# Performance work log

Hardware: AMD Instinct MI355X
Metric: run time of the kernel (lower is better)

Reference implementation:

```python
import jax, jax.numpy as jnp
import numpy as np

H, W, D, EMB, CELL = 16, 16, 6, 32, 128


def mat2quat(m):
    # m: [..., 12] row-major flattened [R|t] (3x4). Branchless vectorized
    # version of the original per-element Python-loop mat2quat.
    trans = m[..., jnp.array([3, 7, 11])]
    m00, m01, m02 = m[..., 0], m[..., 1], m[..., 2]
    m10, m11, m12 = m[..., 4], m[..., 5], m[..., 6]
    m20, m21, m22 = m[..., 8], m[..., 9], m[..., 10]
    t0 = 1 + m00 - m11 - m22
    q0 = jnp.stack([t0, m01 + m10, m20 + m02, m12 - m21], -1)
    t1 = 1 - m00 + m11 - m22
    q1 = jnp.stack([m01 + m10, t1, m12 + m21, m20 - m02], -1)
    t2 = 1 - m00 - m11 + m22
    q2 = jnp.stack([m20 + m02, m12 + m21, t2, m01 - m10], -1)
    t3 = 1 + m00 + m11 + m22
    q3 = jnp.stack([m12 - m21, m20 - m02, m01 - m10, t3], -1)
    cneg, cA, cB = m22 < 0, m00 > m11, m00 < -m11
    t = jnp.where(cneg, jnp.where(cA, t0, t1), jnp.where(cB, t2, t3))
    q = jnp.where(cneg[..., None], jnp.where(cA[..., None], q0, q1),
                  jnp.where(cB[..., None], q2, q3))
    q = q * (0.5 / jnp.sqrt(t))[..., None]
    return jnp.concatenate([trans, q], -1)  # [..., 7]


def transform_pose(pose_o, pose_q):
    # relative pose: inv([R_o|t_o]) @ [R_q|t_q]; original runs under no_grad
    B, N = pose_o.shape[:2]
    aff = jnp.array([0., 0., 0., 1.], dtype=pose_o.dtype)
    mo = jnp.concatenate([pose_o, jnp.broadcast_to(aff, (B, N, 4))], -1).reshape(B, N, 4, 4)
    mq = jnp.concatenate([pose_q, jnp.broadcast_to(aff, (B, 1, 4))], -1).reshape(B, 1, 4, 4)
    mt = jnp.linalg.inv(mo) @ mq  # [B,N,4,4]
    return jax.lax.stop_gradient(mt.reshape(B, N, 16)[..., :12])


def _mlp(x, W1, b1, W2, b2):
    return jax.nn.relu(x @ W1 + b1) @ W2 + b2


def reference(view_cell, pose_o, pose_q, Wk1, bk1, Wk2, bk2,
              Wq1, bq1, Wq2, bq2, Wa1, ba1, Wa2, ba2):
    B, N = pose_o.shape[:2]
    pose_o_quat = mat2quat(pose_o)  # [B,N,7]
    pose_q_quat = mat2quat(pose_q)  # [B,1,7]
    hg, wg = jnp.meshgrid(jnp.linspace(-1., 1., H), jnp.linspace(-1., 1., W), indexing='ij')
    code_o = jnp.stack([hg, wg], -1).reshape(-1, 2)              # [H*W, 2]
    emb_o = _mlp(code_o, Wk1, bk1, Wk2, bk2)                     # [H*W, EMB], shared keys
    dg, hg2, wg2 = jnp.meshgrid(jnp.linspace(0., 1., D), jnp.linspace(-1., 1., H),
                                jnp.linspace(-1., 1., W), indexing='ij')
    code_q = jnp.stack([dg, hg2, wg2], -1).reshape(-1, 3)        # [Q,3], Q=D*H*W
    Q = code_q.shape[0]
    pose_trans = transform_pose(pose_o, pose_q).reshape(B * N, 12)
    inp_q = jnp.concatenate([
        jnp.broadcast_to(pose_trans[:, None, :], (B * N, Q, 12)),
        jnp.broadcast_to(code_q[None], (B * N, Q, 3))], -1)      # [BN,Q,15]
    emb_q = _mlp(inp_q, Wq1, bq1, Wq2, bq2)                      # [BN,Q,EMB]
    mask = jax.nn.sigmoid(_mlp(emb_q, Wa1, ba1, Wa2, ba2))       # [BN,Q,1]
    v = jnp.transpose(view_cell, (0, 2, 3, 1)).reshape(B * N, H * W, CELL)
    att = jax.nn.softmax(jnp.einsum('bqe,ke->bqk', emb_q, emb_o), axis=-1)
    vatt = jnp.einsum('bqk,bkc->bqc', att, v)                    # [BN,Q,CELL]
    fused = jax.nn.sigmoid((mask * vatt).reshape(B, N, Q, CELL).sum(1))  # 'ocm' fusion
    out = jnp.transpose(fused, (0, 2, 1)).reshape(B, CELL, D, H, W)
    return out, pose_o_quat, pose_q_quat


def setup_inputs():
    key = jax.random.key(0)
    ks = jax.random.split(key, 12)
    B, N = 32, 8

    def make_pose(k, shape):
        kq, kt = jax.random.split(k)
        q = jax.random.normal(kq, shape + (4,))
        q = q / jnp.linalg.norm(q, axis=-1, keepdims=True)
        w, x, y, z = q[..., 0], q[..., 1], q[..., 2], q[..., 3]
        R = jnp.stack([1 - 2 * (y * y + z * z), 2 * (x * y - w * z), 2 * (x * z + w * y),
                       2 * (x * y + w * z), 1 - 2 * (x * x + z * z), 2 * (y * z - w * x),
                       2 * (x * z - w * y), 2 * (y * z + w * x), 1 - 2 * (x * x + y * y)],
                      -1).reshape(shape + (3, 3))
        t = jax.random.normal(kt, shape + (3, 1))
        return jnp.concatenate([R, t], -1).reshape(shape + (12,))

    def glorot(k, shp):
        return jax.random.normal(k, shp) * (1.0 / np.sqrt(shp[0]))

    return dict(
        view_cell=jax.random.normal(ks[0], (B * N, CELL, H, W)),
        pose_o=make_pose(ks[1], (B, N)),
        pose_q=make_pose(ks[2], (B, 1)),
        Wk1=glorot(ks[3], (2, 128)), bk1=jnp.zeros(128),
        Wk2=glorot(ks[4], (128, EMB)), bk2=jnp.zeros(EMB),
        Wq1=glorot(ks[5], (15, 256)), bq1=jnp.zeros(256),
        Wq2=glorot(ks[6], (256, EMB)), bq2=jnp.zeros(EMB),
        Wa1=glorot(ks[7], (EMB, 64)), ba1=jnp.zeros(64),
        Wa2=glorot(ks[8], (64, 1)), ba2=jnp.zeros(1),
    )
```

## Files before the change

kernel.cpp:

```cpp
#include <hip/hip_runtime.h>
#include <hip/hip_bf16.h>

using bf16 = __hip_bfloat16;
typedef __bf16 bfrag __attribute__((ext_vector_type(8)));
typedef float  ffrag __attribute__((ext_vector_type(4)));

#define WS_EO    0
#define WS_W2T   16384
#define WS_W1T   32768
#define WS_WA1T  49152
#define WS_VBF   65536

__device__ __forceinline__ float sigmoidf_(float x){ return 1.f/(1.f+__expf(-x)); }

__device__ __forceinline__ void relpose(const float* mo, const float* mq, float* o) {
  float a=mo[0],bb=mo[1],c=mo[2], d=mo[4],e=mo[5],f=mo[6], g=mo[8],h=mo[9],i9=mo[10];
  float A = e*i9-f*h, Bc = f*g-d*i9, C = d*h-e*g;
  float inv = 1.f/(a*A + bb*Bc + c*C);
  float r00=A*inv,  r01=(c*h-bb*i9)*inv, r02=(bb*f-c*e)*inv;
  float r10=Bc*inv, r11=(a*i9-c*g)*inv,  r12=(c*d-a*f)*inv;
  float r20=C*inv,  r21=(bb*g-a*h)*inv,  r22=(a*e-bb*d)*inv;
  float tx = mq[3]-mo[3], ty = mq[7]-mo[7], tz = mq[11]-mo[11];
  o[0]=r00*mq[0]+r01*mq[4]+r02*mq[8];  o[1]=r00*mq[1]+r01*mq[5]+r02*mq[9];
  o[2]=r00*mq[2]+r01*mq[6]+r02*mq[10]; o[3]=r00*tx+r01*ty+r02*tz;
  o[4]=r10*mq[0]+r11*mq[4]+r12*mq[8];  o[5]=r10*mq[1]+r11*mq[5]+r12*mq[9];
  o[6]=r10*mq[2]+r11*mq[6]+r12*mq[10]; o[7]=r10*tx+r11*ty+r12*tz;
  o[8]=r20*mq[0]+r21*mq[4]+r22*mq[8];  o[9]=r20*mq[1]+r21*mq[5]+r22*mq[9];
  o[10]=r20*mq[2]+r21*mq[6]+r22*mq[10]; o[11]=r20*tx+r21*ty+r22*tz;
}

__device__ __forceinline__ void quat7(const float* m, float* o) {
  float m00=m[0], m01=m[1], m02=m[2];
  float m10=m[4], m11=m[5], m12=m[6];
  float m20=m[8], m21=m[9], m22=m[10];
  float t,q0,q1,q2,q3;
  if (m22 < 0.f) {
    if (m00 > m11) { t=1.f+m00-m11-m22; q0=t;        q1=m01+m10; q2=m20+m02; q3=m12-m21; }
    else           { t=1.f-m00+m11-m22; q0=m01+m10; q1=t;        q2=m12+m21; q3=m20-m02; }
  } else {
    if (m00 < -m11){ t=1.f-m00-m11+m22; q0=m20+m02; q1=m12+m21; q2=t;        q3=m01-m10; }
    else           { t=1.f+m00+m11+m22; q0=m12-m21; q1=m20-m02; q2=m01-m10; q3=t;        }
  }
  float s = 0.5f / sqrtf(t);
  o[0]=m[3]; o[1]=m[7]; o[2]=m[11];
// ... 50 lines not shown
      for (int u=0;u<8;u++) {
        float4 w = *(const float4*)&Wk2[j*32+u*4];
        acc[u*4+0] = fmaf(hj, w.x, acc[u*4+0]);
        acc[u*4+1] = fmaf(hj, w.y, acc[u*4+1]);
        acc[u*4+2] = fmaf(hj, w.z, acc[u*4+2]);
        acc[u*4+3] = fmaf(hj, w.w, acc[u*4+3]);
      }
    }
    #pragma unroll
    for (int e=0;e<32;e++) ws_eo[k*32+e] = __float2bfloat16(acc[e]);
  } else if (role == 2) {
    int k = tid;
    #pragma unroll
    for (int u=0;u<8;u++) {
      float4 w = *(const float4*)&Wq2[k*32+u*4];
      ws_w2t[(u*4+0)*256+k] = __float2bfloat16(w.x);
      ws_w2t[(u*4+1)*256+k] = __float2bfloat16(w.y);
      ws_w2t[(u*4+2)*256+k] = __float2bfloat16(w.z);
      ws_w2t[(u*4+3)*256+k] = __float2bfloat16(w.w);
    }
  } else if (role == 3) {
    int h = tid;
    bf16 row[32];
    #pragma unroll
    for (int i=0;i<15;i++) row[i] = __float2bfloat16(Wq1[i*256+h]);
    row[15] = __float2bfloat16(bq1[h]);
    #pragma unroll
    for (int i=16;i<32;i++) row[i] = __float2bfloat16(0.f);
    #pragma unroll
    for (int i=0;i<32;i++) ws_w1t[h*32+i] = row[i];
  } else {
    if (tid < 64) {
      #pragma unroll
      for (int e=0;e<32;e++) ws_wa1t[tid*32+e] = __float2bfloat16(Wa1[e*64+tid]);
    }
  }
}

template<bool PRE>
__global__ void __launch_bounds__(256, 3)
k_main(const float* __restrict__ vc, const bf16* __restrict__ vbf_,
       const float* __restrict__ pose_o, const float* __restrict__ pose_q,
       const bf16* __restrict__ ws_eo_, const bf16* __restrict__ ws_w2t_,
       const bf16* __restrict__ ws_w1t_, const bf16* __restrict__ ws_wa1t_,
       const float* __restrict__ bq2,
       const float* __restrict__ ba1, const float* __restrict__ Wa2,
       const float* __restrict__ ba2,
       float* __restrict__ out) {
  __shared__ __align__(16) __bf16 s_h[32*264];
  __shared__ __align__(16) __bf16 s_p[32*264];
  __shared__ __align__(16) __bf16 s_eqT[32*40];
  __shared__ float s_pt[8][12];
  __shared__ float s_bw[128];
  __shared__ float s_redA[2][16][4];
  __shared__ float s_redB[2][16][4];
  __shared__ float s_redC[2][16][4];

  const __bf16* vbf  = (const __bf16*)vbf_;
  const __bf16* eo   = (const __bf16*)ws_eo_;
  const __bf16* w2t  = (const __bf16*)ws_w2t_;
  const __bf16* w1t  = (const __bf16*)ws_w1t_;
  const __bf16* wa1t = (const __bf16*)ws_wa1t_;

  const int tid  = threadIdx.x;
  const int w    = tid >> 6;
  const int lane = tid & 63;
  const int quad = lane >> 4;
  const int l15  = lane & 15;
  const int b    = blockIdx.y;
  const int qt0  = blockIdx.x * 32;

  if (tid < 8) {
    float mo[12], mq[12], pt[12];
    #pragma unroll
    for (int i=0;i<12;i++) mo[i] = pose_o[(b*8+tid)*12+i];
    #pragma unroll
    for (int i=0;i<12;i++) mq[i] = pose_q[b*12+i];
    relpose(mo, mq, pt);
    #pragma unroll
    for (int i=0;i<12;i++) s_pt[tid][i] = pt[i];
  }
  if (tid < 64) s_bw[tid] = ba1[tid];
  else if (tid < 128) s_bw[tid] = Wa2[tid-64];
  __syncthreads();

  bfrag w1A[4], eoA[4], waA;
  #pragma unroll
  for (int t=0;t<4;t++) {
    w1A[t] = *(const bfrag*)&w1t[((w*4+t)*16+l15)*32 + quad*8];
    eoA[t] = *(const bfrag*)&eo[((w*4+t)*16+l15)*32 + quad*8];
  }
  waA = *(const bfrag*)&wa1t[(w*16+l15)*32 + quad*8];
  const int   qs2 = w & 1, et = w >> 1;
  const float bq2v = bq2[et*16 + l15];
  float ba1r[4], wa2r[4];
  #pragma unroll
  for (int r=0;r<4;r++) { ba1r[r] = s_bw[w*16+quad*4+r]; wa2r[r] = s_bw[64+w*16+quad*4+r]; }
  const float ba2v = ba2[0];
  float c012[2][3];
  #pragma unroll
  for (int qs=0;qs<2;qs++) {
    int qg = qt0 + qs*16 + l15;
    c012[qs][0] = (float)(qg>>8) * 0.2f;
    c012[qs][1] = -1.f + (float)((qg>>4)&15)*(2.f/15.f);
    c012[qs][2] = -1.f + (float)(qg&15)*(2.f/15.f);
  }

  float acc[2][2][4];
  #pragma unroll
  for (int ct=0;ct<2;ct++)
    #pragma unroll
    for (int qs=0;qs<2;qs++)
      #pragma unroll
      for (int r=0;r<4;r++) acc[ct][qs][r] = 0.f;

  #pragma unroll 1
  for (int n=0; n<8; n++) {
    const int bn = b*8 + n;
    {
      bfrag Bx[2];
      #pragma unroll
      for (int qs=0;qs<2;qs++) {
        #pragma unroll
        for (int j=0;j<8;j++) {
          int k = quad*8+j;
          float v = (k<12) ? s_pt[n][k<12?k:0]
                  : (k==12) ? c012[qs][0] : (k==13) ? c012[qs][1]
                  : (k==14) ? c012[qs][2] : (k==15) ? 1.f : 0.f;
          Bx[qs][j] = (__bf16)v;
        }
      }
      #pragma unroll
      for (int t=0;t<4;t++) {
        #pragma unroll
        for (int qs=0;qs<2;qs++) {
          ffrag C = {0.f,0.f,0.f,0.f};
          C = __builtin_amdgcn_mfma_f32_16x16x32_bf16(w1A[t], Bx[qs], C, 0, 0, 0);
          __bf16 p[4] __attribute__((aligned(8)));
          #pragma unroll
          for (int r=0;r<4;r++) p[r] = (__bf16)fmaxf(C[r], 0.f);
          *(uint2*)&s_h[(qs*16+l15)*264 + (w*4+t)*16 + quad*4] = *(const uint2*)p;
        }
      }
    }
    __syncthreads();
    {
      ffrag C2 = {0.f,0.f,0.f,0.f};
      #pragma unroll
      for (int s=0;s<8;s++) {
        bfrag A  = *(const bfrag*)&s_h[(qs2*16+l15)*264 + s*32 + quad*8];
        bfrag Bw = *(const bfrag*)&w2t[(et*16+l15)*256 + s*32 + quad*8];
        C2 = __builtin_amdgcn_mfma_f32_16x16x32_bf16(A, Bw, C2, 0, 0, 0);
      }
      #pragma unroll
      for (int r=0;r<4;r++)
        s_eqT[(qs2*16+quad*4+r)*40 + et*16 + l15] = (__bf16)(C2[r] + bq2v);
    }
    __syncthreads();
    bfrag Bq[2];
    Bq[0] = *(const bfrag*)&s_eqT[l15*40 + quad*8];
    Bq[1] = *(const bfrag*)&s_eqT[(16+l15)*40 + quad*8];
    float S[2][4][4];
    #pragma unroll
    for (int t=0;t<4;t++) {
      #pragma unroll
      for (int qs=0;qs<2;qs++) {
        ffrag C = {0.f,0.f,0.f,0.f};
        C = __builtin_amdgcn_mfma_f32_16x16x32_bf16(eoA[t], Bq[qs], C, 0, 0, 0);
        #pragma unroll
        for (int r=0;r<4;r++) S[qs][t][r] = C[r];
      }
    }
    #pragma unroll
    for (int qs=0;qs<2;qs++) {
      ffrag Cm = {0.f,0.f,0.f,0.f};
      Cm = __builtin_amdgcn_mfma_f32_16x16x32_bf16(waA, Bq[qs], Cm, 0, 0, 0);
      float msum = 0.f;
      #pragma unroll
      for (int r=0;r<4;r++) msum += fmaxf(Cm[r] + ba1r[r], 0.f) * wa2r[r];
      msum += __shfl_xor(msum, 16);
      msum += __shfl_xor(msum, 32);
      float mx = -1e30f;
      #pragma unroll
      for (int t=0;t<4;t++)
        #pragma unroll
        for (int r=0;r<4;r++) mx = fmaxf(mx, S[qs][t][r]);
      mx = fmaxf(mx, __shfl_xor(mx, 16));
      mx = fmaxf(mx, __shfl_xor(mx, 32));
      if (quad == 0) { s_redA[qs][l15][w] = msum; s_redB[qs][l15][w] = mx; }
    }
    __syncthreads();
    #pragma unroll
    for (int qs=0;qs<2;qs++) {
      float rmax = fmaxf(fmaxf(s_redB[qs][l15][0], s_redB[qs][l15][1]),
                         fmaxf(s_redB[qs][l15][2], s_redB[qs][l15][3]));
      float sum = 0.f;
      #pragma unroll
      for (int t=0;t<4;t++) {
        __bf16 p[4] __attribute__((aligned(8)));
        #pragma unroll
        for (int r=0;r<4;r++) { float e = __expf(S[qs][t][r]-rmax); sum += e; p[r] = (__bf16)e; }
        *(uint2*)&s_p[(qs*16+l15)*264 + (w*4+t)*16 + quad*4] = *(const uint2*)p;
      }
      sum += __shfl_xor(sum, 16);
      sum += __shfl_xor(sum, 32);
      if (quad == 0) s_redC[qs][l15][w] = sum;
    }
    __syncthreads();
    float rs[2];
    #pragma unroll
    for (int qs=0;qs<2;qs++) {
      float msumT = ba2v + s_redA[qs][l15][0] + s_redA[qs][l15][1]
                         + s_redA[qs][l15][2] + s_redA[qs][l15][3];
      float ssum  = s_redC[qs][l15][0] + s_redC[qs][l15][1]
                  + s_redC[qs][l15][2] + s_redC[qs][l15][3];
      rs[qs] = sigmoidf_(msumT) / ssum;
    }
    {
      ffrag Cv[2][2];
      #pragma unroll
      for (int ct=0;ct<2;ct++)
        #pragma unroll
        for (int qs=0;qs<2;qs++) Cv[ct][qs] = (ffrag){0.f,0.f,0.f,0.f};
      #pragma unroll
      for (int s=0;s<8;s++) {
        bfrag Bp0 = *(const bfrag*)&s_p[l15*264 + s*32 + quad*8];
        bfrag Bp1 = *(const bfrag*)&s_p[(16+l15)*264 + s*32 + quad*8];
        #pragma unroll
        for (int ct=0;ct<2;ct++) {
          bfrag Av;
          if (PRE) {
            Av = *(const bfrag*)&vbf[((size_t)bn<<15) + ((2*w+ct)*16+l15)*256 + s*32 + quad*8];
          } else {
            const float* p0 = &vc[((size_t)bn<<15) + ((2*w+ct)*16+l15)*256 + s*32 + quad*8];
            float4 a0 = *(const float4*)p0, a1 = *(const float4*)(p0+4);
            Av[0]=(__bf16)a0.x; Av[1]=(__bf16)a0.y; Av[2]=(__bf16)a0.z; Av[3]=(__bf16)a0.w;
            Av[4]=(__bf16)a1.x; Av[5]=(__bf16)a1.y; Av[6]=(__bf16)a1.z; Av[7]=(__bf16)a1.w;
          }
          Cv[ct][0] = __builtin_amdgcn_mfma_f32_16x16x32_bf16(Av, Bp0, Cv[ct][0], 0, 0, 0);
          Cv[ct][1] = __builtin_amdgcn_mfma_f32_16x16x32_bf16(Av, Bp1, Cv[ct][1], 0, 0, 0);
        }
      }
      #pragma unroll
      for (int ct=0;ct<2;ct++)
        #pragma unroll
        for (int qs=0;qs<2;qs++)
          #pragma unroll
          for (int r=0;r<4;r++) acc[ct][qs][r] = fmaf(rs[qs], Cv[ct][qs][r], acc[ct][qs][r]);
    }
    __syncthreads();
  }
  #pragma unroll
  for (int ct=0;ct<2;ct++) {
    #pragma unroll
    for (int qs=0;qs<2;qs++) {
      #pragma unroll
      for (int r=0;r<4;r++) {
        int c = (2*w+ct)*16 + quad*4 + r;
        out[(size_t)b*196608 + (size_t)c*1536 + qt0 + qs*16 + l15] = sigmoidf_(acc[ct][qs][r]);
      }
    }
  }
}

extern "C" void kernel_launch(void* const* d_in, const int* in_sizes, int n_in,
                              void* d_out, int out_size, void* d_ws, size_t ws_size,
                              hipStream_t stream) {
  const float* view_cell = (const float*)d_in[0];
  const float* pose_o = (const float*)d_in[1];
  const float* pose_q = (const float*)d_in[2];
  const float* Wk1 = (const float*)d_in[3];
  const float* bk1 = (const float*)d_in[4];
  const float* Wk2 = (const float*)d_in[5];
  const float* bk2 = (const float*)d_in[6];
  const float* Wq1 = (const float*)d_in[7];
  const float* bq1 = (const float*)d_in[8];
  const float* Wq2 = (const float*)d_in[9];
  const float* bq2 = (const float*)d_in[10];
  const float* Wa1 = (const float*)d_in[11];
  const float* ba1 = (const float*)d_in[12];
  const float* Wa2 = (const float*)d_in[13];
  const float* ba2 = (const float*)d_in[14];

  float* out = (float*)d_out;
  float* out_qo = out + 6291456;
  float* out_qq = out + 6291456 + 1792;

  bf16* ws_eo   = (bf16*)((char*)d_ws + WS_EO);
  bf16* ws_w2t  = (bf16*)((char*)d_ws + WS_W2T);
  bf16* ws_w1t  = (bf16*)((char*)d_ws + WS_W1T);
  bf16* ws_wa1t = (bf16*)((char*)d_ws + WS_WA1T);
  bf16* ws_vbf  = (bf16*)((char*)d_ws + WS_VBF);

  const bool pre = ws_size >= (size_t)(WS_VBF + 256u*128u*256u*2u);
  const int vblocks = pre ? 4096 : 0;

  hipLaunchKernelGGL(k_prep, dim3(vblocks + 5), dim3(256), 0, stream,
                     view_cell, ws_vbf, pose_o, pose_q, Wk1, bk1, Wk2, bk2,
                     Wq1, bq1, Wq2, Wa1, out_qo, out_qq,
                     ws_eo, ws_w2t, ws_w1t, ws_wa1t, vblocks);

  if (pre) {
    hipLaunchKernelGGL((k_main<true>), dim3(48, 32), dim3(256), 0, stream,
                       view_cell, ws_vbf, pose_o, pose_q, ws_eo, ws_w2t,
                       ws_w1t, ws_wa1t, bq2, ba1, Wa2, ba2, out);
  } else {
    hipLaunchKernelGGL((k_main<false>), dim3(48, 32), dim3(256), 0, stream,
                       view_cell, ws_vbf, pose_o, pose_q, ws_eo, ws_w2t,
                       ws_w1t, ws_wa1t, bq2, ba1, Wa2, ba2, out);
  }
}
```

Before: 256.1 us.

## Collapse main kernel to single-wave blocks, removing cross-wave syncs and shared reductions

Each block of k_main becomes one 64-lane wavefront that computes all 256 hidden units, all 16 key tiles and all 128 output channels itself. This removes the block-wide barriers and the shared-memory reductions for max, sum and gate, and merges the two shared buffers into one. The softmax moves to exp2 by folding log2(e) into the query bias and query output, with a matching ln2 factor on Wa1. The trade-off is more registers per thread (acc grows to 8x2 fragments) and weight fragments reloaded inside the loop. Blocks and occupancy also change: 1536 blocks of 64 threads instead of 1536 blocks of 256.

```diff
diff --git a/kernel.cpp b/kernel.cpp
--- a/kernel.cpp
+++ b/kernel.cpp
@@ -10,6 +10,9 @@
 #define WS_W1T   32768
 #define WS_WA1T  49152
 #define WS_VBF   65536
+
+#define LOG2E 1.44269504f
+#define LN2   0.6931471805599453f
 
 __device__ __forceinline__ float sigmoidf_(float x){ return 1.f/(1.f+__expf(-x)); }
 
@@ -126,13 +129,13 @@
   } else {
     if (tid < 64) {
       #pragma unroll
-      for (int e=0;e<32;e++) ws_wa1t[tid*32+e] = __float2bfloat16(Wa1[e*64+tid]);
+      for (int e=0;e<32;e++) ws_wa1t[tid*32+e] = __float2bfloat16(Wa1[e*64+tid] * LN2);
     }
   }
 }
 
 template<bool PRE>
-__global__ void __launch_bounds__(256, 3)
+__global__ void __launch_bounds__(64, 2)
 k_main(const float* __restrict__ vc, const bf16* __restrict__ vbf_,
        const float* __restrict__ pose_o, const float* __restrict__ pose_q,
        const bf16* __restrict__ ws_eo_, const bf16* __restrict__ ws_w2t_,
@@ -141,14 +144,9 @@
        const float* __restrict__ ba1, const float* __restrict__ Wa2,
        const float* __restrict__ ba2,
        float* __restrict__ out) {
-  __shared__ __align__(16) __bf16 s_h[32*264];
-  __shared__ __align__(16) __bf16 s_p[32*264];
-  __shared__ __align__(16) __bf16 s_eqT[32*40];
-  __shared__ float s_pt[8][12];
-  __shared__ float s_bw[128];
-  __shared__ float s_redA[2][16][4];
-  __shared__ float s_redB[2][16][4];
-  __shared__ float s_redC[2][16][4];
+  __shared__ __align__(16) __bf16 s_hp[32*264];
+  __shared__ __align__(16) __bf16 s_eq[32*40];
+  __shared__ __align__(16) float  s_pt[96];
 
   const __bf16* vbf  = (const __bf16*)vbf_;
   const __bf16* eo   = (const __bf16*)ws_eo_;
@@ -156,41 +154,24 @@
   const __bf16* w1t  = (const __bf16*)ws_w1t_;
   const __bf16* wa1t = (const __bf16*)ws_wa1t_;
 
-  const int tid  = threadIdx.x;
-  const int w    = tid >> 6;
-  const int lane = tid & 63;
+  const int lane = threadIdx.x;
   const int quad = lane >> 4;
   const int l15  = lane & 15;
-  const int b    = blockIdx.y;
-  const int qt0  = blockIdx.x * 32;
-
-  if (tid < 8) {
+  const int b    = blockIdx.x & 31;
+  const int qt0  = (blockIdx.x >> 5) * 32;
+
+  if (lane < 8) {
     float mo[12], mq[12], pt[12];
     #pragma unroll
-    for (int i=0;i<12;i++) mo[i] = pose_o[(b*8+tid)*12+i];
+    for (int i=0;i<12;i++) mo[i] = pose_o[(b*8+lane)*12+i];
     #pragma unroll
     for (int i=0;i<12;i++) mq[i] = pose_q[b*12+i];
     relpose(mo, mq, pt);
     #pragma unroll
-    for (int i=0;i<12;i++) s_pt[tid][i] = pt[i];
-  }
-  if (tid < 64) s_bw[tid] = ba1[tid];
-  else if (tid < 128) s_bw[tid] = Wa2[tid-64];
+    for (int i=0;i<12;i++) s_pt[lane*12+i] = pt[i];
+  }
   __syncthreads();
 
-  bfrag w1A[4], eoA[4], waA;
-  #pragma unroll
-  for (int t=0;t<4;t++) {
-    w1A[t] = *(const bfrag*)&w1t[((w*4+t)*16+l15)*32 + quad*8];
-    eoA[t] = *(const bfrag*)&eo[((w*4+t)*16+l15)*32 + quad*8];
-  }
-  waA = *(const bfrag*)&wa1t[(w*16+l15)*32 + quad*8];
-  const int   qs2 = w & 1, et = w >> 1;
-  const float bq2v = bq2[et*16 + l15];
-  float ba1r[4], wa2r[4];
-  #pragma unroll
-  for (int r=0;r<4;r++) { ba1r[r] = s_bw[w*16+quad*4+r]; wa2r[r] = s_bw[64+w*16+quad*4+r]; }
-  const float ba2v = ba2[0];
   float c012[2][3];
   #pragma unroll
   for (int qs=0;qs<2;qs++) {
@@ -199,158 +180,178 @@
     c012[qs][1] = -1.f + (float)((qg>>4)&15)*(2.f/15.f);
     c012[qs][2] = -1.f + (float)(qg&15)*(2.f/15.f);
   }
-
-  float acc[2][2][4];
+  const float bq2s0 = bq2[l15]    * LOG2E;
+  const float bq2s1 = bq2[16+l15] * LOG2E;
+  const float ba2v  = ba2[0];
+
+  ffrag acc[8][2];
   #pragma unroll
-  for (int ct=0;ct<2;ct++)
-    #pragma unroll
-    for (int qs=0;qs<2;qs++)
-      #pragma unroll
-      for (int r=0;r<4;r++) acc[ct][qs][r] = 0.f;
+  for (int ct=0;ct<8;ct++) {
+    acc[ct][0] = (ffrag){0.f,0.f,0.f,0.f};
+    acc[ct][1] = (ffrag){0.f,0.f,0.f,0.f};
+  }
 
   #pragma unroll 1
   for (int n=0; n<8; n++) {
     const int bn = b*8 + n;
     {
+      float4 pa = *(const float4*)&s_pt[n*12];
+      float4 pb = *(const float4*)&s_pt[n*12+4];
+      float4 pc = *(const float4*)&s_pt[n*12+8];
       bfrag Bx[2];
       #pragma unroll
       for (int qs=0;qs<2;qs++) {
-        #pragma unroll
-        for (int j=0;j<8;j++) {
-          int k = quad*8+j;
-          float v = (k<12) ? s_pt[n][k<12?k:0]
-                  : (k==12) ? c012[qs][0] : (k==13) ? c012[qs][1]
-                  : (k==14) ? c012[qs][2] : (k==15) ? 1.f : 0.f;
-          Bx[qs][j] = (__bf16)v;
+        bfrag x;
+        if (quad == 0) {
+          x[0]=(__bf16)pa.x; x[1]=(__bf16)pa.y; x[2]=(__bf16)pa.z; x[3]=(__bf16)pa.w;
+          x[4]=(__bf16)pb.x; x[5]=(__bf16)pb.y; x[6]=(__bf16)pb.z; x[7]=(__bf16)pb.w;
+        } else if (quad == 1) {
+          x[0]=(__bf16)pc.x; x[1]=(__bf16)pc.y; x[2]=(__bf16)pc.z; x[3]=(__bf16)pc.w;
+          x[4]=(__bf16)c012[qs][0]; x[5]=(__bf16)c012[qs][1];
+          x[6]=(__bf16)c012[qs][2]; x[7]=(__bf16)1.f;
+        } else {
+          #pragma unroll
+          for (int j=0;j<8;j++) x[j]=(__bf16)0.f;
         }
-      }
-      #pragma unroll
-      for (int t=0;t<4;t++) {
+        Bx[qs] = x;
+      }
+      #pragma unroll
+      for (int t=0;t<16;t++) {
+        bfrag A = *(const bfrag*)&w1t[(t*16+l15)*32 + quad*8];
         #pragma unroll
         for (int qs=0;qs<2;qs++) {
           ffrag C = {0.f,0.f,0.f,0.f};
-          C = __builtin_amdgcn_mfma_f32_16x16x32_bf16(w1A[t], Bx[qs], C, 0, 0, 0);
+          C = __builtin_amdgcn_mfma_f32_16x16x32_bf16(A, Bx[qs], C, 0, 0, 0);
           __bf16 p[4] __attribute__((aligned(8)));
           #pragma unroll
           for (int r=0;r<4;r++) p[r] = (__bf16)fmaxf(C[r], 0.f);
-          *(uint2*)&s_h[(qs*16+l15)*264 + (w*4+t)*16 + quad*4] = *(const uint2*)p;
+          *(uint2*)&s_hp[(qs*16+l15)*264 + t*16 + quad*4] = *(const uint2*)p;
         }
       }
     }
-    __syncthreads();
     {
-      ffrag C2 = {0.f,0.f,0.f,0.f};
+      ffrag C2[2][2];
+      C2[0][0]=(ffrag){0.f,0.f,0.f,0.f}; C2[0][1]=(ffrag){0.f,0.f,0.f,0.f};
+      C2[1][0]=(ffrag){0.f,0.f,0.f,0.f}; C2[1][1]=(ffrag){0.f,0.f,0.f,0.f};
       #pragma unroll
       for (int s=0;s<8;s++) {
-        bfrag A  = *(const bfrag*)&s_h[(qs2*16+l15)*264 + s*32 + quad*8];
-        bfrag Bw = *(const bfrag*)&w2t[(et*16+l15)*256 + s*32 + quad*8];
-        C2 = __builtin_amdgcn_mfma_f32_16x16x32_bf16(A, Bw, C2, 0, 0, 0);
-      }
-      #pragma unroll
-      for (int r=0;r<4;r++)
-        s_eqT[(qs2*16+quad*4+r)*40 + et*16 + l15] = (__bf16)(C2[r] + bq2v);
-    }
-    __syncthreads();
-    bfrag Bq[2];
-    Bq[0] = *(const bfrag*)&s_eqT[l15*40 + quad*8];
-    Bq[1] = *(const bfrag*)&s_eqT[(16+l15)*40 + quad*8];
-    float S[2][4][4];
-    #pragma unroll
-    for (int t=0;t<4;t++) {
-      #pragma unroll
-      for (int qs=0;qs<2;qs++) {
-        ffrag C = {0.f,0.f,0.f,0.f};
-        C = __builtin_amdgcn_mfma_f32_16x16x32_bf16(eoA[t], Bq[qs], C, 0, 0, 0);
+        bfrag A0 = *(const bfrag*)&s_hp[l15*264      + s*32 + quad*8];
+        bfrag A1 = *(const bfrag*)&s_hp[(16+l15)*264 + s*32 + quad*8];
+        bfrag B0 = *(const bfrag*)&w2t[l15*256      + s*32 + quad*8];
+        bfrag B1 = *(const bfrag*)&w2t[(16+l15)*256 + s*32 + quad*8];
+        C2[0][0] = __builtin_amdgcn_mfma_f32_16x16x32_bf16(A0, B0, C2[0][0], 0, 0, 0);
+        C2[0][1] = __builtin_amdgcn_mfma_f32_16x16x32_bf16(A0, B1, C2[0][1], 0, 0, 0);
+        C2[1][0] = __builtin_amdgcn_mfma_f32_16x16x32_bf16(A1, B0, C2[1][0], 0, 0, 0);
+        C2[1][1] = __builtin_amdgcn_mfma_f32_16x16x32_bf16(A1, B1, C2[1][1], 0, 0, 0);
+      }
+      #pragma unroll
+      for (int qs=0;qs<2;qs++)
         #pragma unroll
-        for (int r=0;r<4;r++) S[qs][t][r] = C[r];
-      }
-    }
+        for (int et=0;et<2;et++)
+          #pragma unroll
+          for (int r=0;r<4;r++) {
+            float es = fmaf(C2[qs][et][r], LOG2E, et ? bq2s1 : bq2s0);
+            s_eq[(qs*16+quad*4+r)*40 + et*16 + l15] = (__bf16)es;
+          }
+    }
+    bfrag Bq0 = *(const bfrag*)&s_eq[l15*40      + quad*8];
+    bfrag Bq1 = *(const bfrag*)&s_eq[(16+l15)*40 + quad*8];
+    float msum0 = 0.f, msum1 = 0.f;
+    #pragma unroll
+    for (int ut=0; ut<4; ut++) {
+      bfrag Aw = *(const bfrag*)&wa1t[(ut*16+l15)*32 + quad*8];
+      ffrag Cm0 = {0.f,0.f,0.f,0.f}, Cm1 = {0.f,0.f,0.f,0.f};
+      Cm0 = __builtin_amdgcn_mfma_f32_16x16x32_bf16(Aw, Bq0, Cm0, 0, 0, 0);
+      Cm1 = __builtin_amdgcn_mfma_f32_16x16x32_bf16(Aw, Bq1, Cm1, 0, 0, 0);
+      float4 bav = *(const float4*)&ba1[ut*16 + quad*4];
+      float4 wav = *(const float4*)&Wa2[ut*16 + quad*4];
+      msum0 = fmaf(fmaxf(Cm0[0]+bav.x,0.f), wav.x, msum0);
+      msum0 = fmaf(fmaxf(Cm0[1]+bav.y,0.f), wav.y, msum0);
+      msum0 = fmaf(fmaxf(Cm0[2]+bav.z,0.f), wav.z, msum0);
+      msum0 = fmaf(fmaxf(Cm0[3]+bav.w,0.f), wav.w, msum0);
+      msum1 = fmaf(fmaxf(Cm1[0]+bav.x,0.f), wav.x, msum1);
+      msum1 = fmaf(fmaxf(Cm1[1]+bav.y,0.f), wav.y, msum1);
+      msum1 = fmaf(fmaxf(Cm1[2]+bav.z,0.f), wav.z, msum1);
+      msum1 = fmaf(fmaxf(Cm1[3]+bav.w,0.f), wav.w, msum1);
+    }
+    msum0 += __shfl_xor(msum0, 16); msum0 += __shfl_xor(msum0, 32);
+    msum1 += __shfl_xor(msum1, 16); msum1 += __shfl_xor(msum1, 32);
+    float rs0, rs1;
     #pragma unroll
     for (int qs=0;qs<2;qs++) {
-      ffrag Cm = {0.f,0.f,0.f,0.f};
-      Cm = __builtin_amdgcn_mfma_f32_16x16x32_bf16(waA, Bq[qs], Cm, 0, 0, 0);
-      float msum = 0.f;
-      #pragma unroll
-      for (int r=0;r<4;r++) msum += fmaxf(Cm[r] + ba1r[r], 0.f) * wa2r[r];
-      msum += __shfl_xor(msum, 16);
-      msum += __shfl_xor(msum, 32);
+      const bfrag Bq = qs ? Bq1 : Bq0;
+      ffrag Sv[16];
       float mx = -1e30f;
       #pragma unroll
-      for (int t=0;t<4;t++)
-        #pragma unroll
-        for (int r=0;r<4;r++) mx = fmaxf(mx, S[qs][t][r]);
+      for (int t=0;t<16;t++) {
+        bfrag Ae = *(const bfrag*)&eo[(t*16+l15)*32 + quad*8];
+        ffrag S = {0.f,0.f,0.f,0.f};
+        S = __builtin_amdgcn_mfma_f32_16x16x32_bf16(Ae, Bq, S, 0, 0, 0);
+        Sv[t] = S;
+        mx = fmaxf(mx, fmaxf(fmaxf(S[0], S[1]), fmaxf(S[2], S[3])));
+      }
       mx = fmaxf(mx, __shfl_xor(mx, 16));
       mx = fmaxf(mx, __shfl_xor(mx, 32));
-      if (quad == 0) { s_redA[qs][l15][w] = msum; s_redB[qs][l15][w] = mx; }
-    }
-    __syncthreads();
-    #pragma unroll
-    for (int qs=0;qs<2;qs++) {
-      float rmax = fmaxf(fmaxf(s_redB[qs][l15][0], s_redB[qs][l15][1]),
-                         fmaxf(s_redB[qs][l15][2], s_redB[qs][l15][3]));
-      float sum = 0.f;
-      #pragma unroll
-      for (int t=0;t<4;t++) {
+      float ps = 0.f;
+      #pragma unroll
+      for (int t=0;t<16;t++) {
         __bf16 p[4] __attribute__((aligned(8)));
         #pragma unroll
-        for (int r=0;r<4;r++) { float e = __expf(S[qs][t][r]-rmax); sum += e; p[r] = (__bf16)e; }
-        *(uint2*)&s_p[(qs*16+l15)*264 + (w*4+t)*16 + quad*4] = *(const uint2*)p;
-      }
-      sum += __shfl_xor(sum, 16);
-      sum += __shfl_xor(sum, 32);
-      if (quad == 0) s_redC[qs][l15][w] = sum;
-    }
-    __syncthreads();
-    float rs[2];
-    #pragma unroll
-    for (int qs=0;qs<2;qs++) {
-      float msumT = ba2v + s_redA[qs][l15][0] + s_redA[qs][l15][1]
-                         + s_redA[qs][l15][2] + s_redA[qs][l15][3];
-      float ssum  = s_redC[qs][l15][0] + s_redC[qs][l15][1]
-                  + s_redC[qs][l15][2] + s_redC[qs][l15][3];
-      rs[qs] = sigmoidf_(msumT) / ssum;
-    }
-    {
-      ffrag Cv[2][2];
-      #pragma unroll
-      for (int ct=0;ct<2;ct++)
+        for (int r=0;r<4;r++) {
+          float e = exp2f(Sv[t][r] - mx);
+          ps += e;
+          p[r] = (__bf16)e;
+        }
+        *(uint2*)&s_hp[(qs*16+l15)*264 + t*16 + quad*4] = *(const uint2*)p;
+      }
+      ps += __shfl_xor(ps, 16); ps += __shfl_xor(ps, 32);
+      float rsv = sigmoidf_((qs ? msum1 : msum0) + ba2v) / ps;
+      if (qs == 0) rs0 = rsv; else rs1 = rsv;
+    }
+    #pragma unroll
+    for (int g=0; g<2; g++) {
+      ffrag Cv[4][2];
+      #pragma unroll
+      for (int c4=0;c4<4;c4++) {
+        Cv[c4][0] = (ffrag){0.f,0.f,0.f,0.f};
+        Cv[c4][1] = (ffrag){0.f,0.f,0.f,0.f};
+      }
+      #pragma unroll
+      for (int s=0;s<8;s++) {
+        bfrag Bp0 = *(const bfrag*)&s_hp[l15*264      + s*32 + quad*8];
+        bfrag Bp1 = *(const bfrag*)&s_hp[(16+l15)*264 + s*32 + quad*8];
         #pragma unroll
-        for (int qs=0;qs<2;qs++) Cv[ct][qs] = (ffrag){0.f,0.f,0.f,0.f};
-      #pragma unroll
-      for (int s=0;s<8;s++) {
-        bfrag Bp0 = *(const bfrag*)&s_p[l15*264 + s*32 + quad*8];
-        bfrag Bp1 = *(const bfrag*)&s_p[(16+l15)*264 + s*32 + quad*8];
-        #pragma unroll
-        for (int ct=0;ct<2;ct++) {
+        for (int c4=0;c4<4;c4++) {
+          int ct = g*4 + c4;
           bfrag Av;
           if (PRE) {
-            Av = *(const bfrag*)&vbf[((size_t)bn<<15) + ((2*w+ct)*16+l15)*256 + s*32 + quad*8];
+            Av = *(const bfrag*)&vbf[((size_t)bn<<15) + (ct*16+l15)*256 + s*32 + quad*8];
           } else {
-            const float* p0 = &vc[((size_t)bn<<15) + ((2*w+ct)*16+l15)*256 + s*32 + quad*8];
+            const float* p0 = &vc[((size_t)bn<<15) + (ct*16+l15)*256 + s*32 + quad*8];
             float4 a0 = *(const float4*)p0, a1 = *(const float4*)(p0+4);
             Av[0]=(__bf16)a0.x; Av[1]=(__bf16)a0.y; Av[2]=(__bf16)a0.z; Av[3]=(__bf16)a0.w;
             Av[4]=(__bf16)a1.x; Av[5]=(__bf16)a1.y; Av[6]=(__bf16)a1.z; Av[7]=(__bf16)a1.w;
           }
-          Cv[ct][0] = __builtin_amdgcn_mfma_f32_16x16x32_bf16(Av, Bp0, Cv[ct][0], 0, 0, 0);
-          Cv[ct][1] = __builtin_amdgcn_mfma_f32_16x16x32_bf16(Av, Bp1, Cv[ct][1], 0, 0, 0);
+          Cv[c4][0] = __builtin_amdgcn_mfma_f32_16x16x32_bf16(Av, Bp0, Cv[c4][0], 0, 0, 0);
+          Cv[c4][1] = __builtin_amdgcn_mfma_f32_16x16x32_bf16(Av, Bp1, Cv[c4][1], 0, 0, 0);
         }
       }
       #pragma unroll
-      for (int ct=0;ct<2;ct++)
+      for (int c4=0;c4<4;c4++)
         #pragma unroll
-        for (int qs=0;qs<2;qs++)
-          #pragma unroll
-          for (int r=0;r<4;r++) acc[ct][qs][r] = fmaf(rs[qs], Cv[ct][qs][r], acc[ct][qs][r]);
-    }
-    __syncthreads();
+        for (int r=0;r<4;r++) {
+          acc[g*4+c4][0][r] = fmaf(rs0, Cv[c4][0][r], acc[g*4+c4][0][r]);
+          acc[g*4+c4][1][r] = fmaf(rs1, Cv[c4][1][r], acc[g*4+c4][1][r]);
+        }
+    }
   }
   #pragma unroll
-  for (int ct=0;ct<2;ct++) {
+  for (int ct=0;ct<8;ct++) {
     #pragma unroll
     for (int qs=0;qs<2;qs++) {
       #pragma unroll
       for (int r=0;r<4;r++) {
-        int c = (2*w+ct)*16 + quad*4 + r;
+        int c = ct*16 + quad*4 + r;
         out[(size_t)b*196608 + (size_t)c*1536 + qt0 + qs*16 + l15] = sigmoidf_(acc[ct][qs][r]);
       }
     }
@@ -395,11 +396,11 @@
                      ws_eo, ws_w2t, ws_w1t, ws_wa1t, vblocks);
 
   if (pre) {
-    hipLaunchKernelGGL((k_main<true>), dim3(48, 32), dim3(256), 0, stream,
+    hipLaunchKernelGGL((k_main<true>), dim3(1536), dim3(64), 0, stream,
                        view_cell, ws_vbf, pose_o, pose_q, ws_eo, ws_w2t,
                        ws_w1t, ws_wa1t, bq2, ba1, Wa2, ba2, out);
   } else {
-    hipLaunchKernelGGL((k_main<false>), dim3(48, 32), dim3(256), 0, stream,
+    hipLaunchKernelGGL((k_main<false>), dim3(1536), dim3(64), 0, stream,
                        view_cell, ws_vbf, pose_o, pose_q, ws_eo, ws_w2t,
                        ws_w1t, ws_wa1t, bq2, ba1, Wa2, ba2, out);
   }
```

After: 390.3 us. +52.4%, slower.

## Software-pipeline attention loop: overlap value MFMA of view n-1 with query MLP

Applied to the files above, without the earlier changes.

Restructures the per-view loop into a one-stage software pipeline. The value-weighted MFMA accumulation for view n-1 now runs in the same iteration as the query MLP and score computation for view n. The hidden and probability buffers are merged into a double-buffered shared array, and one barrier per iteration is dropped. Softmax switches from exp to exp2 by folding log2(e) into the query embedding output, with Wa1 prescaled by ln2 to compensate. This aims to hide global-load latency and cut sync count, at the cost of more live registers and some bf16 rounding differences.

```diff
diff --git a/kernel.cpp b/kernel.cpp
--- a/kernel.cpp
+++ b/kernel.cpp
@@ -10,6 +10,9 @@
 #define WS_W1T   32768
 #define WS_WA1T  49152
 #define WS_VBF   65536
+
+#define LOG2E 1.44269504f
+#define LN2   0.6931471805599453f
 
 __device__ __forceinline__ float sigmoidf_(float x){ return 1.f/(1.f+__expf(-x)); }
 
@@ -126,7 +129,7 @@
   } else {
     if (tid < 64) {
       #pragma unroll
-      for (int e=0;e<32;e++) ws_wa1t[tid*32+e] = __float2bfloat16(Wa1[e*64+tid]);
+      for (int e=0;e<32;e++) ws_wa1t[tid*32+e] = __float2bfloat16(Wa1[e*64+tid] * LN2);
     }
   }
 }
@@ -141,8 +144,7 @@
        const float* __restrict__ ba1, const float* __restrict__ Wa2,
        const float* __restrict__ ba2,
        float* __restrict__ out) {
-  __shared__ __align__(16) __bf16 s_h[32*264];
-  __shared__ __align__(16) __bf16 s_p[32*264];
+  __shared__ __align__(16) __bf16 s_hp[2][32*264];
   __shared__ __align__(16) __bf16 s_eqT[32*40];
   __shared__ float s_pt[8][12];
   __shared__ float s_bw[128];
@@ -186,7 +188,7 @@
   }
   waA = *(const bfrag*)&wa1t[(w*16+l15)*32 + quad*8];
   const int   qs2 = w & 1, et = w >> 1;
-  const float bq2v = bq2[et*16 + l15];
+  const float bq2v = bq2[et*16 + l15] * LOG2E;
   float ba1r[4], wa2r[4];
   #pragma unroll
   for (int r=0;r<4;r++) { ba1r[r] = s_bw[w*16+quad*4+r]; wa2r[r] = s_bw[64+w*16+quad*4+r]; }
@@ -207,11 +209,13 @@
     for (int qs=0;qs<2;qs++)
       #pragma unroll
       for (int r=0;r<4;r++) acc[ct][qs][r] = 0.f;
+  float rs_prev[2] = {0.f, 0.f};
 
   #pragma unroll 1
-  for (int n=0; n<8; n++) {
-    const int bn = b*8 + n;
-    {
+  for (int n=0; n<=8; n++) {
+    __bf16* H        = s_hp[n&1];
+    const __bf16* Hp = s_hp[(n+1)&1];
+    if (n < 8) {
       bfrag Bx[2];
       #pragma unroll
       for (int qs=0;qs<2;qs++) {
@@ -233,84 +237,25 @@
           __bf16 p[4] __attribute__((aligned(8)));
           #pragma unroll
           for (int r=0;r<4;r++) p[r] = (__bf16)fmaxf(C[r], 0.f);
-          *(uint2*)&s_h[(qs*16+l15)*264 + (w*4+t)*16 + quad*4] = *(const uint2*)p;
+          *(uint2*)&H[(qs*16+l15)*264 + (w*4+t)*16 + quad*4] = *(const uint2*)p;
         }
       }
     }
     __syncthreads();
-    {
+    if (n < 8) {
       ffrag C2 = {0.f,0.f,0.f,0.f};
       #pragma unroll
       for (int s=0;s<8;s++) {
-        bfrag A  = *(const bfrag*)&s_h[(qs2*16+l15)*264 + s*32 + quad*8];
+        bfrag A  = *(const bfrag*)&H[(qs2*16+l15)*264 + s*32 + quad*8];
         bfrag Bw = *(const bfrag*)&w2t[(et*16+l15)*256 + s*32 + quad*8];
         C2 = __builtin_amdgcn_mfma_f32_16x16x32_bf16(A, Bw, C2, 0, 0, 0);
       }
       #pragma unroll
       for (int r=0;r<4;r++)
-        s_eqT[(qs2*16+quad*4+r)*40 + et*16 + l15] = (__bf16)(C2[r] + bq2v);
-    }
-    __syncthreads();
-    bfrag Bq[2];
-    Bq[0] = *(const bfrag*)&s_eqT[l15*40 + quad*8];
-    Bq[1] = *(const bfrag*)&s_eqT[(16+l15)*40 + quad*8];
-    float S[2][4][4];
-    #pragma unroll
-    for (int t=0;t<4;t++) {
-      #pragma unroll
-      for (int qs=0;qs<2;qs++) {
-        ffrag C = {0.f,0.f,0.f,0.f};
-        C = __builtin_amdgcn_mfma_f32_16x16x32_bf16(eoA[t], Bq[qs], C, 0, 0, 0);
-        #pragma unroll
-        for (int r=0;r<4;r++) S[qs][t][r] = C[r];
-      }
-    }
-    #pragma unroll
-    for (int qs=0;qs<2;qs++) {
-      ffrag Cm = {0.f,0.f,0.f,0.f};
-      Cm = __builtin_amdgcn_mfma_f32_16x16x32_bf16(waA, Bq[qs], Cm, 0, 0, 0);
-      float msum = 0.f;
-      #pragma unroll
-      for (int r=0;r<4;r++) msum += fmaxf(Cm[r] + ba1r[r], 0.f) * wa2r[r];
-      msum += __shfl_xor(msum, 16);
-      msum += __shfl_xor(msum, 32);
-      float mx = -1e30f;
-      #pragma unroll
-      for (int t=0;t<4;t++)
-        #pragma unroll
-        for (int r=0;r<4;r++) mx = fmaxf(mx, S[qs][t][r]);
-      mx = fmaxf(mx, __shfl_xor(mx, 16));
-      mx = fmaxf(mx, __shfl_xor(mx, 32));
-      if (quad == 0) { s_redA[qs][l15][w] = msum; s_redB[qs][l15][w] = mx; }
-    }
-    __syncthreads();
-    #pragma unroll
-    for (int qs=0;qs<2;qs++) {
-      float rmax = fmaxf(fmaxf(s_redB[qs][l15][0], s_redB[qs][l15][1]),
-                         fmaxf(s_redB[qs][l15][2], s_redB[qs][l15][3]));
-      float sum = 0.f;
-      #pragma unroll
-      for (int t=0;t<4;t++) {
-        __bf16 p[4] __attribute__((aligned(8)));
-        #pragma unroll
-        for (int r=0;r<4;r++) { float e = __expf(S[qs][t][r]-rmax); sum += e; p[r] = (__bf16)e; }
-        *(uint2*)&s_p[(qs*16+l15)*264 + (w*4+t)*16 + quad*4] = *(const uint2*)p;
-      }
-      sum += __shfl_xor(sum, 16);
-      sum += __shfl_xor(sum, 32);
-      if (quad == 0) s_redC[qs][l15][w] = sum;
-    }
-    __syncthreads();
-    float rs[2];
-    #pragma unroll
-    for (int qs=0;qs<2;qs++) {
-      float msumT = ba2v + s_redA[qs][l15][0] + s_redA[qs][l15][1]
-                         + s_redA[qs][l15][2] + s_redA[qs][l15][3];
-      float ssum  = s_redC[qs][l15][0] + s_redC[qs][l15][1]
-                  + s_redC[qs][l15][2] + s_redC[qs][l15][3];
-      rs[qs] = sigmoidf_(msumT) / ssum;
-    }
-    {
+        s_eqT[(qs2*16+quad*4+r)*40 + et*16 + l15] = (__bf16)fmaf(C2[r], LOG2E, bq2v);
+    }
+    if (n > 0) {
+      const int bnp = b*8 + (n-1);
       ffrag Cv[2][2];
       #pragma unroll
       for (int ct=0;ct<2;ct++)
@@ -318,15 +263,15 @@
         for (int qs=0;qs<2;qs++) Cv[ct][qs] = (ffrag){0.f,0.f,0.f,0.f};
       #pragma unroll
       for (int s=0;s<8;s++) {
-        bfrag Bp0 = *(const bfrag*)&s_p[l15*264 + s*32 + quad*8];
-        bfrag Bp1 = *(const bfrag*)&s_p[(16+l15)*264 + s*32 + quad*8];
+        bfrag Bp0 = *(const bfrag*)&Hp[l15*264 + s*32 + quad*8];
+        bfrag Bp1 = *(const bfrag*)&Hp[(16+l15)*264 + s*32 + quad*8];
         #pragma unroll
         for (int ct=0;ct<2;ct++) {
           bfrag Av;
           if (PRE) {
-            Av = *(const bfrag*)&vbf[((size_t)bn<<15) + ((2*w+ct)*16+l15)*256 + s*32 + quad*8];
+            Av = *(const bfrag*)&vbf[((size_t)bnp<<15) + ((2*w+ct)*16+l15)*256 + s*32 + quad*8];
           } else {
-            const float* p0 = &vc[((size_t)bn<<15) + ((2*w+ct)*16+l15)*256 + s*32 + quad*8];
+            const float* p0 = &vc[((size_t)bnp<<15) + ((2*w+ct)*16+l15)*256 + s*32 + quad*8];
             float4 a0 = *(const float4*)p0, a1 = *(const float4*)(p0+4);
             Av[0]=(__bf16)a0.x; Av[1]=(__bf16)a0.y; Av[2]=(__bf16)a0.z; Av[3]=(__bf16)a0.w;
             Av[4]=(__bf16)a1.x; Av[5]=(__bf16)a1.y; Av[6]=(__bf16)a1.z; Av[7]=(__bf16)a1.w;
@@ -340,9 +285,69 @@
         #pragma unroll
         for (int qs=0;qs<2;qs++)
           #pragma unroll
-          for (int r=0;r<4;r++) acc[ct][qs][r] = fmaf(rs[qs], Cv[ct][qs][r], acc[ct][qs][r]);
-    }
-    __syncthreads();
+          for (int r=0;r<4;r++) acc[ct][qs][r] = fmaf(rs_prev[qs], Cv[ct][qs][r], acc[ct][qs][r]);
+    }
+    if (n < 8) {
+      __syncthreads();
+      bfrag Bq[2];
+      Bq[0] = *(const bfrag*)&s_eqT[l15*40 + quad*8];
+      Bq[1] = *(const bfrag*)&s_eqT[(16+l15)*40 + quad*8];
+      float S[2][4][4];
+      #pragma unroll
+      for (int t=0;t<4;t++) {
+        #pragma unroll
+        for (int qs=0;qs<2;qs++) {
+          ffrag C = {0.f,0.f,0.f,0.f};
+          C = __builtin_amdgcn_mfma_f32_16x16x32_bf16(eoA[t], Bq[qs], C, 0, 0, 0);
+          #pragma unroll
+          for (int r=0;r<4;r++) S[qs][t][r] = C[r];
+        }
+      }
+      #pragma unroll
+      for (int qs=0;qs<2;qs++) {
+        ffrag Cm = {0.f,0.f,0.f,0.f};
+        Cm = __builtin_amdgcn_mfma_f32_16x16x32_bf16(waA, Bq[qs], Cm, 0, 0, 0);
+        float msum = 0.f;
+        #pragma unroll
+        for (int r=0;r<4;r++) msum += fmaxf(Cm[r] + ba1r[r], 0.f) * wa2r[r];
+        msum += __shfl_xor(msum, 16);
+        msum += __shfl_xor(msum, 32);
+        float mx = -1e30f;
+        #pragma unroll
+        for (int t=0;t<4;t++)
+          #pragma unroll
+          for (int r=0;r<4;r++) mx = fmaxf(mx, S[qs][t][r]);
+        mx = fmaxf(mx, __shfl_xor(mx, 16));
+        mx = fmaxf(mx, __shfl_xor(mx, 32));
+        if (quad == 0) { s_redA[qs][l15][w] = msum; s_redB[qs][l15][w] = mx; }
+      }
+      __syncthreads();
+      #pragma unroll
+      for (int qs=0;qs<2;qs++) {
+        float rmax = fmaxf(fmaxf(s_redB[qs][l15][0], s_redB[qs][l15][1]),
+                           fmaxf(s_redB[qs][l15][2], s_redB[qs][l15][3]));
+        float sum = 0.f;
+        #pragma unroll
+        for (int t=0;t<4;t++) {
+          __bf16 p[4] __attribute__((aligned(8)));
+          #pragma unroll
+          for (int r=0;r<4;r++) { float e = exp2f(S[qs][t][r]-rmax); sum += e; p[r] = (__bf16)e; }
+          *(uint2*)&H[(qs*16+l15)*264 + (w*4+t)*16 + quad*4] = *(const uint2*)p;
+        }
+        sum += __shfl_xor(sum, 16);
+        sum += __shfl_xor(sum, 32);
+        if (quad == 0) s_redC[qs][l15][w] = sum;
+      }
+      __syncthreads();
+      #pragma unroll
+      for (int qs=0;qs<2;qs++) {
+        float msumT = ba2v + s_redA[qs][l15][0] + s_redA[qs][l15][1]
+                           + s_redA[qs][l15][2] + s_redA[qs][l15][3];
+        float ssum  = s_redC[qs][l15][0] + s_redC[qs][l15][1]
+                    + s_redC[qs][l15][2] + s_redC[qs][l15][3];
+        rs_prev[qs] = sigmoidf_(msumT) / ssum;
+      }
+    }
   }
   #pragma unroll
   for (int ct=0;ct<2;ct++) {
```

After: 291.1 us. +13.7%, slower.

## Prefetch view tiles at loop start and fold log2e scaling for exp2 softmax

Applied to the files above, without the earlier changes.

When the bf16 view tensor is precomputed, its tiles for each view are loaded into registers at the top of the per-view loop, so the global-memory latency overlaps with the pose MLP and softmax stages. Softmax uses exp2f, with LOG2E folded into the query embedding and ln2 into Wa1 so the attention-gate logit is unchanged. The pose input row is stored as packed bf16 and assembled with vector selects. The second MLP matmul is split into two independent accumulator chains. The register prefetch raises VGPR pressure under launch_bounds(256,3), which may cause spills or lower occupancy.

```diff
diff --git a/kernel.cpp b/kernel.cpp
--- a/kernel.cpp
+++ b/kernel.cpp
@@ -4,12 +4,18 @@
 using bf16 = __hip_bfloat16;
 typedef __bf16 bfrag __attribute__((ext_vector_type(8)));
 typedef float  ffrag __attribute__((ext_vector_type(4)));
+typedef unsigned int u32;
+typedef u32 u32x4 __attribute__((ext_vector_type(4)));
+typedef u32 u32x2 __attribute__((ext_vector_type(2)));
 
 #define WS_EO    0
 #define WS_W2T   16384
 #define WS_W1T   32768
 #define WS_WA1T  49152
 #define WS_VBF   65536
+
+#define LOG2E 1.44269504f
+#define LN2   0.6931471805599453f
 
 __device__ __forceinline__ float sigmoidf_(float x){ return 1.f/(1.f+__expf(-x)); }
 
@@ -126,7 +132,7 @@
   } else {
     if (tid < 64) {
       #pragma unroll
-      for (int e=0;e<32;e++) ws_wa1t[tid*32+e] = __float2bfloat16(Wa1[e*64+tid]);
+      for (int e=0;e<32;e++) ws_wa1t[tid*32+e] = __float2bfloat16(Wa1[e*64+tid] * LN2);
     }
   }
 }
@@ -144,7 +150,7 @@
   __shared__ __align__(16) __bf16 s_h[32*264];
   __shared__ __align__(16) __bf16 s_p[32*264];
   __shared__ __align__(16) __bf16 s_eqT[32*40];
-  __shared__ float s_pt[8][12];
+  __shared__ __align__(16) __bf16 s_ptb[8][16];
   __shared__ float s_bw[128];
   __shared__ float s_redA[2][16][4];
   __shared__ float s_redB[2][16][4];
@@ -172,7 +178,9 @@
     for (int i=0;i<12;i++) mq[i] = pose_q[b*12+i];
     relpose(mo, mq, pt);
     #pragma unroll
-    for (int i=0;i<12;i++) s_pt[tid][i] = pt[i];
+    for (int i=0;i<12;i++) s_ptb[tid][i] = (__bf16)pt[i];
+    #pragma unroll
+    for (int i=12;i<16;i++) s_ptb[tid][i] = (__bf16)0.f;
   }
   if (tid < 64) s_bw[tid] = ba1[tid];
   else if (tid < 128) s_bw[tid] = Wa2[tid-64];
@@ -186,19 +194,26 @@
   }
   waA = *(const bfrag*)&wa1t[(w*16+l15)*32 + quad*8];
   const int   qs2 = w & 1, et = w >> 1;
-  const float bq2v = bq2[et*16 + l15];
+  const float bq2v = bq2[et*16 + l15] * LOG2E;
   float ba1r[4], wa2r[4];
   #pragma unroll
   for (int r=0;r<4;r++) { ba1r[r] = s_bw[w*16+quad*4+r]; wa2r[r] = s_bw[64+w*16+quad*4+r]; }
   const float ba2v = ba2[0];
-  float c012[2][3];
+  u32x2 tail[2];
   #pragma unroll
   for (int qs=0;qs<2;qs++) {
     int qg = qt0 + qs*16 + l15;
-    c012[qs][0] = (float)(qg>>8) * 0.2f;
-    c012[qs][1] = -1.f + (float)((qg>>4)&15)*(2.f/15.f);
-    c012[qs][2] = -1.f + (float)(qg&15)*(2.f/15.f);
-  }
+    __bf16 t4[4] __attribute__((aligned(8)));
+    t4[0] = (__bf16)((float)(qg>>8) * 0.2f);
+    t4[1] = (__bf16)(-1.f + (float)((qg>>4)&15)*(2.f/15.f));
+    t4[2] = (__bf16)(-1.f + (float)(qg&15)*(2.f/15.f));
+    t4[3] = (__bf16)1.f;
+    tail[qs] = *(const u32x2*)t4;
+  }
+  const bool isq0 = (quad == 0), isq1 = (quad == 1);
+
+  const __bf16* vb0 = vbf + (((size_t)b*8)<<15) + (size_t)((2*w*16+l15)*256 + quad*8);
+  const __bf16* vb1 = vb0 + 16*256;
 
   float acc[2][2][4];
   #pragma unroll
@@ -210,19 +225,27 @@
 
   #pragma unroll 1
   for (int n=0; n<8; n++) {
-    const int bn = b*8 + n;
+    bfrag Vp0[8], Vp1[8];
+    if (PRE) {
+      const __bf16* p0 = vb0 + ((size_t)n<<15);
+      const __bf16* p1 = vb1 + ((size_t)n<<15);
+      #pragma unroll
+      for (int s=0;s<8;s++) Vp0[s] = *(const bfrag*)(p0 + s*32);
+      #pragma unroll
+      for (int s=0;s<8;s++) Vp1[s] = *(const bfrag*)(p1 + s*32);
+    }
     {
+      u32x4 rowlo = *(const u32x4*)&s_ptb[n][0];
+      u32x2 rowhi = *(const u32x2*)&s_ptb[n][8];
       bfrag Bx[2];
       #pragma unroll
       for (int qs=0;qs<2;qs++) {
-        #pragma unroll
-        for (int j=0;j<8;j++) {
-          int k = quad*8+j;
-          float v = (k<12) ? s_pt[n][k<12?k:0]
-                  : (k==12) ? c012[qs][0] : (k==13) ? c012[qs][1]
-                  : (k==14) ? c012[qs][2] : (k==15) ? 1.f : 0.f;
-          Bx[qs][j] = (__bf16)v;
-        }
+        union { u32x4 u; bfrag f; } bx;
+        bx.u.x = isq0 ? rowlo.x : (isq1 ? rowhi.x : 0u);
+        bx.u.y = isq0 ? rowlo.y : (isq1 ? rowhi.y : 0u);
+        bx.u.z = isq0 ? rowlo.z : (isq1 ? tail[qs].x : 0u);
+        bx.u.w = isq0 ? rowlo.w : (isq1 ? tail[qs].y : 0u);
+        Bx[qs] = bx.f;
       }
       #pragma unroll
       for (int t=0;t<4;t++) {
@@ -239,16 +262,19 @@
     }
     __syncthreads();
     {
-      ffrag C2 = {0.f,0.f,0.f,0.f};
-      #pragma unroll
-      for (int s=0;s<8;s++) {
-        bfrag A  = *(const bfrag*)&s_h[(qs2*16+l15)*264 + s*32 + quad*8];
-        bfrag Bw = *(const bfrag*)&w2t[(et*16+l15)*256 + s*32 + quad*8];
-        C2 = __builtin_amdgcn_mfma_f32_16x16x32_bf16(A, Bw, C2, 0, 0, 0);
+      ffrag Ca = {0.f,0.f,0.f,0.f}, Cb = {0.f,0.f,0.f,0.f};
+      #pragma unroll
+      for (int s=0;s<4;s++) {
+        bfrag A0 = *(const bfrag*)&s_h[(qs2*16+l15)*264 + s*32 + quad*8];
+        bfrag B0 = *(const bfrag*)&w2t[(et*16+l15)*256 + s*32 + quad*8];
+        bfrag A1 = *(const bfrag*)&s_h[(qs2*16+l15)*264 + (s+4)*32 + quad*8];
+        bfrag B1 = *(const bfrag*)&w2t[(et*16+l15)*256 + (s+4)*32 + quad*8];
+        Ca = __builtin_amdgcn_mfma_f32_16x16x32_bf16(A0, B0, Ca, 0, 0, 0);
+        Cb = __builtin_amdgcn_mfma_f32_16x16x32_bf16(A1, B1, Cb, 0, 0, 0);
       }
       #pragma unroll
       for (int r=0;r<4;r++)
-        s_eqT[(qs2*16+quad*4+r)*40 + et*16 + l15] = (__bf16)(C2[r] + bq2v);
+        s_eqT[(qs2*16+quad*4+r)*40 + et*16 + l15] = (__bf16)fmaf(Ca[r]+Cb[r], LOG2E, bq2v);
     }
     __syncthreads();
     bfrag Bq[2];
@@ -293,7 +319,7 @@
       for (int t=0;t<4;t++) {
         __bf16 p[4] __attribute__((aligned(8)));
         #pragma unroll
-        for (int r=0;r<4;r++) { float e = __expf(S[qs][t][r]-rmax); sum += e; p[r] = (__bf16)e; }
+        for (int r=0;r<4;r++) { float e = exp2f(S[qs][t][r]-rmax); sum += e; p[r] = (__bf16)e; }
         *(uint2*)&s_p[(qs*16+l15)*264 + (w*4+t)*16 + quad*4] = *(const uint2*)p;
       }
       sum += __shfl_xor(sum, 16);
@@ -311,6 +337,7 @@
       rs[qs] = sigmoidf_(msumT) / ssum;
     }
     {
+      const int bn = b*8 + n;
       ffrag Cv[2][2];
       #pragma unroll
       for (int ct=0;ct<2;ct++)
@@ -320,20 +347,24 @@
       for (int s=0;s<8;s++) {
         bfrag Bp0 = *(const bfrag*)&s_p[l15*264 + s*32 + quad*8];
         bfrag Bp1 = *(const bfrag*)&s_p[(16+l15)*264 + s*32 + quad*8];
-        #pragma unroll
-        for (int ct=0;ct<2;ct++) {
-          bfrag Av;
-          if (PRE) {
-            Av = *(const bfrag*)&vbf[((size_t)bn<<15) + ((2*w+ct)*16+l15)*256 + s*32 + quad*8];
-          } else {
-            const float* p0 = &vc[((size_t)bn<<15) + ((2*w+ct)*16+l15)*256 + s*32 + quad*8];
-            float4 a0 = *(const float4*)p0, a1 = *(const float4*)(p0+4);
-            Av[0]=(__bf16)a0.x; Av[1]=(__bf16)a0.y; Av[2]=(__bf16)a0.z; Av[3]=(__bf16)a0.w;
-            Av[4]=(__bf16)a1.x; Av[5]=(__bf16)a1.y; Av[6]=(__bf16)a1.z; Av[7]=(__bf16)a1.w;
-          }
-          Cv[ct][0] = __builtin_amdgcn_mfma_f32_16x16x32_bf16(Av, Bp0, Cv[ct][0], 0, 0, 0);
-          Cv[ct][1] = __builtin_amdgcn_mfma_f32_16x16x32_bf16(Av, Bp1, Cv[ct][1], 0, 0, 0);
+        bfrag Av0, Av1;
+        if (PRE) {
+          Av0 = Vp0[s];
+          Av1 = Vp1[s];
+        } else {
+          const float* p0 = &vc[((size_t)bn<<15) + ((2*w+0)*16+l15)*256 + s*32 + quad*8];
+          const float* p1 = &vc[((size_t)bn<<15) + ((2*w+1)*16+l15)*256 + s*32 + quad*8];
+          float4 a0 = *(const float4*)p0, a1 = *(const float4*)(p0+4);
+          Av0[0]=(__bf16)a0.x; Av0[1]=(__bf16)a0.y; Av0[2]=(__bf16)a0.z; Av0[3]=(__bf16)a0.w;
+          Av0[4]=(__bf16)a1.x; Av0[5]=(__bf16)a1.y; Av0[6]=(__bf16)a1.z; Av0[7]=(__bf16)a1.w;
+          float4 b0 = *(const float4*)p1, b1 = *(const float4*)(p1+4);
+          Av1[0]=(__bf16)b0.x; Av1[1]=(__bf16)b0.y; Av1[2]=(__bf16)b0.z; Av1[3]=(__bf16)b0.w;
+          Av1[4]=(__bf16)b1.x; Av1[5]=(__bf16)b1.y; Av1[6]=(__bf16)b1.z; Av1[7]=(__bf16)b1.w;
         }
+        Cv[0][0] = __builtin_amdgcn_mfma_f32_16x16x32_bf16(Av0, Bp0, Cv[0][0], 0, 0, 0);
+        Cv[0][1] = __builtin_amdgcn_mfma_f32_16x16x32_bf16(Av0, Bp1, Cv[0][1], 0, 0, 0);
+        Cv[1][0] = __builtin_amdgcn_mfma_f32_16x16x32_bf16(Av1, Bp0, Cv[1][0], 0, 0, 0);
+        Cv[1][1] = __builtin_amdgcn_mfma_f32_16x16x32_bf16(Av1, Bp1, Cv[1][1], 0, 0, 0);
       }
       #pragma unroll
       for (int ct=0;ct<2;ct++)
```

New measurement: 370.7 us. 44.7% more time.
